# Performance work log

Measured on AMD Instinct MI355X. Metric: run time of the kernel, lower is better.

The kernel has to match this reference:

```python
import jax, jax.numpy as jnp
import numpy as np

N = 50000   # nodes
E = 800000  # edges (avg degree 16)
F = 128     # input_nf = output_nf
H = 128     # hidden_nf


def setup_inputs() -> dict:
    key = jax.random.key(0)
    ks = jax.random.split(key, 10)
    # coords: spatial part in [-1, 1], z-coordinate (last dim) in [0.5, 1.5] (must be > 0)
    xz = jax.random.uniform(ks[0], (N, 3), minval=-1.0, maxval=1.0)
    xz = xz.at[:, -1].set(jax.random.uniform(ks[1], (N,), minval=0.5, maxval=1.5))
    h = jax.random.normal(ks[2], (N, F), dtype=jnp.float32)
    row = jax.random.randint(ks[3], (E,), 0, N)
    # guarantee col != row so AdS distance is strictly positive on every edge
    col = (row + 1 + jax.random.randint(ks[4], (E,), 0, N - 1)) % N
    edge_index = jnp.stack([row, col]).astype(jnp.int32)

    def lin(k, fan_in, fan_out):
        return jax.random.normal(k, (fan_in, fan_out), dtype=jnp.float32) / np.float32(np.sqrt(fan_in))

    return {
        "xz": xz,
        "h": h,
        "We1": lin(ks[5], 2 * F + 1, H), "be1": jnp.full((H,), 0.1, jnp.float32),
        "We2": lin(ks[6], H, H),         "be2": jnp.full((H,), 0.1, jnp.float32),
        "Wn1": lin(ks[7], H + F, H),     "bn1": jnp.full((H,), 0.1, jnp.float32),
        "Wn2": lin(ks[8], H, F),         "bn2": jnp.full((F,), 0.1, jnp.float32),
        "edge_index": edge_index,
    }


def reference(xz, h, We1, be1, We2, be2, Wn1, bn1, Wn2, bn2, edge_index):
    row, col = edge_index[0], edge_index[1]
    n = h.shape[0]

    # AdS (hyperbolic upper-half-space) distance between xz[row] and xz[col]:
    # d = arccosh(1 + |p1 - p2|^2 / (2 z1 z2)), z = last coordinate
    diff = xz[row] - xz[col]                                  # [E, 3]
    u = jnp.sum(diff * diff, axis=-1) / (2.0 * xz[row, -1] * xz[col, -1])
    dist = jnp.arccosh(1.0 + u)[:, None]                      # [E, 1]

    # edge model: concat(source, target, radial) -> Linear -> silu -> Linear -> silu
    m = jnp.concatenate([h[row], h[col], dist], axis=1)       # [E, 2F+1]
    m = jax.nn.silu(m @ We1 + be1)                            # [E, H]
    m = jax.nn.silu(m @ We2 + be2)                            # [E, H]

    # segment_mean over destination nodes (row)
    num = jax.ops.segment_sum(m, row, num_segments=n)                          # [N, H]
    den = jax.ops.segment_sum(jnp.ones_like(m), row, num_segments=n)          # [N, H]
    agg = num / jnp.maximum(den, jnp.ones((), den.dtype))

    # node model: concat(h, agg) -> Linear -> silu -> Linear, plus residual
    z = jnp.concatenate([h, agg], axis=1)                     # [N, F+H]
    out = jax.nn.silu(z @ Wn1 + bn1) @ Wn2 + bn2              # [N, F]
    return h + out
```

## Files before the change

kernel.cpp:

```cpp
#include <hip/hip_runtime.h>

#define NN 50000
#define EE 800000
#define NB 196

typedef __bf16 bf16x8 __attribute__((ext_vector_type(8)));
typedef float  f32x4  __attribute__((ext_vector_type(4)));

__device__ __forceinline__ float bf2f(ushort u) {
    union { unsigned int i; float f; } v; v.i = ((unsigned int)u) << 16; return v.f;
}
__device__ __forceinline__ ushort f2bf(float f) {
    union { float f; unsigned int i; } v; v.f = f;
    unsigned int u = v.i;
    return (ushort)((u + 0x7FFFu + ((u >> 16) & 1u)) >> 16);
}
__device__ __forceinline__ ushort f2bf_fast(float f) {
    union { float f; unsigned int i; } v; v.f = f;
    return (ushort)((v.i + 0x8000u) >> 16);
}
__device__ __forceinline__ float silu(float x) {
    return x * __builtin_amdgcn_rcpf(1.0f + __expf(-x));
}

__device__ __forceinline__ bool detect_isf(const ushort* __restrict__ xzu,
                                           int tid, int* scnt) {
    float v = bf2f(xzu[2 * (tid & 255)]);
    bool sane = (v == v) && (fabsf(v) <= 4.0f);
    unsigned long long m = __ballot(sane);
    if ((tid & 63) == 0) scnt[tid >> 6] = __popcll(m);
    __syncthreads();
    int cnt = scnt[0] + scnt[1] + scnt[2] + scnt[3];
    return cnt < 192;
}

__global__ void prep_all_kernel(const void* __restrict__ hsrc, const void* __restrict__ xzsrc,
                                const int* __restrict__ erow,
                                const void* We1, const void* We2,
                                const void* Wn1, const void* Wn2,
                                const void* be1, const void* be2,
                                const void* bn1, const void* bn2,
                                ushort* __restrict__ hb, float* __restrict__ xzf,
                                int* __restrict__ cntI,
                                ushort* __restrict__ We1s, ushort* __restrict__ We2s,
                                ushort* __restrict__ Wn1s, ushort* __restrict__ Wn2s,
                                float* __restrict__ fb, ushort* __restrict__ wlb) {
    __shared__ int scnt[4];
    const int b = blockIdx.x;
    const int tid = threadIdx.x;

    if (b >= 3712 && b < 6837) {
        int e = (b - 3712) * 256 + tid;
        if (e < EE) atomicAdd(&cntI[erow[e]], 1);
        return;
    }

    const bool isf = detect_isf((const ushort*)xzsrc, tid, scnt);

    if (b < 3125) {
        int i = (b * 256 + tid) * 8;
        uint4 o;
        if (isf) {
            const float* s = (const float*)hsrc + i;
            float4 f0 = *(const float4*)s;
            float4 f1 = *(const float4*)(s + 4);
            o.x = (unsigned int)f2bf(f0.x) | ((unsigned int)f2bf(f0.y) << 16);
            o.y = (unsigned int)f2bf(f0.z) | ((unsigned int)f2bf(f0.w) << 16);
            o.z = (unsigned int)f2bf(f1.x) | ((unsigned int)f2bf(f1.y) << 16);
            o.w = (unsigned int)f2bf(f1.z) | ((unsigned int)f2bf(f1.w) << 16);
        } else {
            o = *(const uint4*)((const ushort*)hsrc + i);
        }
        *(uint4*)(hb + i) = o;
    } else if (b < 3712) {
        int i = (b - 3125) * 256 + tid;
        if (i < NN * 3)
            xzf[i] = isf ? ((const float*)xzsrc)[i] : bf2f(((const ushort*)xzsrc)[i]);
    } else {
        int sw = b - 6837;
        if (sw == 48) {
            for (int j = tid; j < 640; j += 256) {
                int which = j >> 7, k = j & 127;
                const void* src = (which == 0) ? be1 : (which == 1) ? be2 :
                                  (which == 2) ? bn1 : (which == 3) ? bn2 : We1;
                size_t idx = (which == 4) ? ((size_t)256 * 128 + k) : (size_t)k;
                float v = isf ? ((const float*)src)[idx] : bf2f(((const ushort*)src)[idx]);
                fb[j] = v;
                if (which == 4) wlb[k] = f2bf(v);
            }
            return;
        }
        int c = sw * 256 + tid;
        const void* src; ushort* dst; int cl;
        if      (c <  4096) { src = We1; dst = We1s; cl = c;         }
        else if (c <  6144) { src = We2; dst = We2s; cl = c - 4096;  }
        else if (c < 10240) { src = Wn1; dst = Wn1s; cl = c - 6144;  }
        else                { src = Wn2; dst = Wn2s; cl = c - 10240; }
        int l = cl & 63, nt = (cl >> 6) & 7, kc = cl >> 9;
        int kbase = kc * 32 + (l >> 4) * 8;
        int n = nt * 16 + (l & 15);
        ushort tmp[8];
#pragma unroll
        for (int j = 0; j < 8; ++j) {
            size_t idx = (size_t)(kbase + j) * 128 + n;
            tmp[j] = isf ? f2bf(((const float*)src)[idx]) : ((const ushort*)src)[idx];
        }
#pragma unroll
        for (int j = 0; j < 8; ++j) dst[(size_t)cl * 8 + j] = tmp[j];
    }
}

__global__ void scanA_kernel(const int* __restrict__ cntI, int* __restrict__ bsum) {
    __shared__ int s[256];
    int t = threadIdx.x;
    int i = blockIdx.x * 256 + t;
    s[t] = (i < NN) ? cntI[i] : 0;
    __syncthreads();
#pragma unroll
    for (int off = 128; off > 0; off >>= 1) {
        if (t < off) s[t] += s[t + off];
        __syncthreads();
    }
    if (t == 0) bsum[blockIdx.x] = s[0];
}

__global__ void scanC_kernel(const int* __restrict__ cntI, const int* __restrict__ bsum,
                             int* __restrict__ rowStart) {
    __shared__ int s[256];
    __shared__ int sbase;
    int t = threadIdx.x;
    int bv = (t < NB) ? bsum[t] : 0;
    s[t] = bv;
    __syncthreads();
    for (int off = 1; off < 256; off <<= 1) {
        int u = (t >= off) ? s[t - off] : 0;
        __syncthreads();
        if (t >= off) s[t] += u;
        __syncthreads();
    }
    if (t == 0) sbase = (blockIdx.x == 0) ? 0 : s[blockIdx.x - 1];
    __syncthreads();
    int i = blockIdx.x * 256 + t;
    int v = (i < NN) ? cntI[i] : 0;
    s[t] = v;
    __syncthreads();
    for (int off = 1; off < 256; off <<= 1) {
        int u = (t >= off) ? s[t - off] : 0;
        __syncthreads();
        if (t >= off) s[t] += u;
        __syncthreads();
    }
    if (i < NN) rowStart[i] = sbase + s[t] - v;
}

__global__ __launch_bounds__(256, 3) void scatter_pq_kernel(
    const ushort* __restrict__ hb, const ushort* __restrict__ We1s,
    const float* __restrict__ fb, ushort* __restrict__ Pp, ushort* __restrict__ Qq,
    const int* __restrict__ erow, const int* __restrict__ ecol,
    const float* __restrict__ xzf, const int* __restrict__ rowStart,
    int* __restrict__ cursor, int2* __restrict__ eS, uint4* __restrict__ aggz) {
    __shared__ __align__(16) ushort sA[8192];
    const int tid = threadIdx.x;

    if (blockIdx.x >= 3907) {
        const uint4 z = make_uint4(0, 0, 0, 0);
        int g0 = (blockIdx.x - 3907) * 256 + tid;
        const int total = NN * 128 * 4 / 16;
        for (int i = g0; i < total; i += 800 * 256) aggz[i] = z;
        return;
    }
    if (blockIdx.x >= 782) {
        int e = (blockIdx.x - 782) * 256 + tid;
        if (e >= EE) return;
        int r = erow[e], c = ecol[e];
        int pos = rowStart[r] + atomicAdd(&cursor[r], 1);
        float4 a = *(const float4*)(xzf + 3 * r);
        float4 b = *(const float4*)(xzf + 3 * c);
        float dx = a.x - b.x, dy = a.y - b.y, dz = a.z - b.z;
        float u = (dx * dx + dy * dy + dz * dz) * __builtin_amdgcn_rcpf(2.0f * a.z * b.z);
        u = fminf(fmaxf(u, 0.0f), 1.0e6f);
        float d = __logf(1.0f + u + sqrtf(u * (u + 2.0f)));
        eS[pos] = make_int2((r << 16) | c, __float_as_int(d));
        return;
    }

    const int lane = tid & 63, w = tid >> 6;
    const int col = lane & 15, quad = lane >> 4;
    const int nt0 = w * 2;
    const int nA = w * 32 + col, nB = nA + 16;
    const float be1A = fb[nA], be1B = fb[nB];
    const int tile = blockIdx.x;
    const int n0 = tile * 64;
#pragma unroll
    for (int i = 0; i < 4; ++i) {
        int node = n0 + lane;
        uint4 v = (node < NN) ? *(const uint4*)(hb + (size_t)node * 128 + (w + 4 * i) * 8)
                              : make_uint4(0, 0, 0, 0);
        *(uint4*)(sA + (((lane >> 4) * 4 + i) * 64 + w * 16 + (lane & 15)) * 8) = v;
    }
    __syncthreads();

    f32x4 accP[4][2] = {}, accQ[4][2] = {};
#pragma unroll
    for (int kc = 0; kc < 4; ++kc) {
        bf16x8 bp0 = *(const bf16x8*)(We1s + ((kc * 8 + nt0)           * 64 + lane) * 8);
        bf16x8 bp1 = *(const bf16x8*)(We1s + ((kc * 8 + nt0 + 1)       * 64 + lane) * 8);
        bf16x8 bq0 = *(const bf16x8*)(We1s + (((kc + 4) * 8 + nt0)     * 64 + lane) * 8);
        bf16x8 bq1 = *(const bf16x8*)(We1s + (((kc + 4) * 8 + nt0 + 1) * 64 + lane) * 8);
#pragma unroll
        for (int g = 0; g < 4; ++g) {
            bf16x8 a = *(const bf16x8*)(sA + ((g * 4 + kc) * 64 + lane) * 8);
            accP[g][0] = __builtin_amdgcn_mfma_f32_16x16x32_bf16(a, bp0, accP[g][0], 0, 0, 0);
            accP[g][1] = __builtin_amdgcn_mfma_f32_16x16x32_bf16(a, bp1, accP[g][1], 0, 0, 0);
            accQ[g][0] = __builtin_amdgcn_mfma_f32_16x16x32_bf16(a, bq0, accQ[g][0], 0, 0, 0);
            accQ[g][1] = __builtin_amdgcn_mfma_f32_16x16x32_bf16(a, bq1, accQ[g][1], 0, 0, 0);
        }
    }
#pragma unroll
    for (int g = 0; g < 4; ++g) {
#pragma unroll
        for (int r = 0; r < 4; ++r) {
            int node = n0 + g * 16 + quad * 4 + r;
            if (node < NN) {
                size_t o = (size_t)node * 128;
                Pp[o + nA] = f2bf(accP[g][0][r] + be1A);
                Pp[o + nB] = f2bf(accP[g][1][r] + be1B);
                Qq[o + nA] = f2bf(accQ[g][0][r]);
                Qq[o + nB] = f2bf(accQ[g][1][r]);
            }
        }
    }
}

__global__ __launch_bounds__(256, 4) void edge_kernel(
    const ushort* __restrict__ Pp, const ushort* __restrict__ Qq,
    const int2* __restrict__ eS, const ushort* __restrict__ We2s,
    const ushort* __restrict__ wlb, const float* __restrict__ fb,
    float* __restrict__ agg) {
    __shared__ __align__(16) char smem[64 * 132 * 4];
    __shared__ int sRow[64];
    ushort* sM = (ushort*)smem;
    float (*sOut)[132] = (float(*)[132])smem;

    const int tid = threadIdx.x;
    const int lane = tid & 63, w = tid >> 6;
    const int col = lane & 15, quad = lane >> 4;
    const int nt0 = w * 2;

    const int nA = w * 32 + col, nB = nA + 16;
    const float be2A = fb[128 + nA], be2B = fb[128 + nB];

    const int ntiles = EE / 64;
    const int per = (ntiles + gridDim.x - 1) / gridDim.x;
    const int t0 = blockIdx.x * per;
    const int t1 = (t0 + per < ntiles) ? (t0 + per) : ntiles;
    if (t0 >= t1) return;

    bf16x8 B2[8];
#pragma unroll
    for (int kc = 0; kc < 4; ++kc) {
        B2[kc * 2]     = *(const bf16x8*)(We2s + ((kc * 8 + nt0)     * 64 + lane) * 8);
        B2[kc * 2 + 1] = *(const bf16x8*)(We2s + ((kc * 8 + nt0 + 1) * 64 + lane) * 8);
    }
    bf16x8 WL[4];
#pragma unroll
    for (int i = 0; i < 4; ++i) WL[i] = *(const bf16x8*)(wlb + (w + 4 * i) * 8);

    int2 ed = eS[(size_t)t0 * 64 + lane];

    for (int tile = t0; tile < t1; ++tile) {
        const int tn = (tile + 1 < t1) ? (tile + 1) : tile;
        const int2 edn = eS[(size_t)tn * 64 + lane];

        __syncthreads();
        const int r = ((unsigned)ed.x) >> 16, c = ed.x & 0xFFFF;
        const float d = __int_as_float(ed.y);
        if (w == 0) sRow[lane] = r;
#pragma unroll
        for (int i = 0; i < 4; ++i) {
            int ch = w + 4 * i;
            bf16x8 p = *(const bf16x8*)(Pp + (size_t)r * 128 + ch * 8);
            bf16x8 q = *(const bf16x8*)(Qq + (size_t)c * 128 + ch * 8);
            ushort out8[8];
#pragma unroll
            for (int j = 0; j < 8; ++j) {
                float x = (float)p[j] + (float)q[j] + d * (float)WL[i][j];
                out8[j] = f2bf_fast(silu(x));
            }
            *(uint4*)(sM + (((lane >> 4) * 4 + i) * 64 + w * 16 + (lane & 15)) * 8) =
                *(const uint4*)out8;
        }
        ed = edn;
        __syncthreads();

        f32x4 acc2[4][2] = {};
#pragma unroll
        for (int kc = 0; kc < 4; ++kc) {
#pragma unroll
            for (int g = 0; g < 4; ++g) {
                bf16x8 a = *(const bf16x8*)(sM + ((g * 4 + kc) * 64 + lane) * 8);
                acc2[g][0] = __builtin_amdgcn_mfma_f32_16x16x32_bf16(a, B2[kc * 2],     acc2[g][0], 0, 0, 0);
                acc2[g][1] = __builtin_amdgcn_mfma_f32_16x16x32_bf16(a, B2[kc * 2 + 1], acc2[g][1], 0, 0, 0);
            }
        }
        __syncthreads();

#pragma unroll
        for (int g = 0; g < 4; ++g) {
#pragma unroll
            for (int r4 = 0; r4 < 4; ++r4) {
                int m = g * 16 + quad * 4 + r4;
                sOut[m][nA] = silu(acc2[g][0][r4] + be2A);
                sOut[m][nB] = silu(acc2[g][1][r4] + be2B);
            }
        }
        __syncthreads();

        {
            const int cc = tid & 127;
            const int mb = (tid >> 7) * 32;
            float acc = 0.0f;
            int prow = sRow[mb];
            for (int k = 0; k < 32; ++k) {
                int rw = sRow[mb + k];
                if (rw != prow) {
                    unsafeAtomicAdd(&agg[(size_t)prow * 128 + cc], acc);
                    acc = 0.0f;
                    prow = rw;
                }
                acc += sOut[mb + k][cc];
            }
            unsafeAtomicAdd(&agg[(size_t)prow * 128 + cc], acc);
        }
    }
}

__global__ __launch_bounds__(256, 3) void node_kernel(
    const ushort* __restrict__ hb, const void* __restrict__ hraw,
    const void* __restrict__ xzsrc,
    const float* __restrict__ agg, const int* __restrict__ cntI,
    const ushort* __restrict__ Wn1s, const ushort* __restrict__ Wn2s,
    const float* __restrict__ fb, void* __restrict__ outv) {
    __shared__ __align__(16) ushort sA[16384];
    __shared__ __align__(16) ushort sM[8192];
    __shared__ int scnt[4];
    const int tid = threadIdx.x;
    const int lane = tid & 63, w = tid >> 6;
    const int col = lane & 15, quad = lane >> 4;
    const int nt0 = w * 2;
    const int ntiles = (NN + 63) / 64;
    const bool isf = detect_isf((const ushort*)xzsrc, tid, scnt);
    float* outf = (float*)outv;
    ushort* outu = (ushort*)outv;

    const int nA = w * 32 + col, nB = nA + 16;
    const float bn1A = fb[256 + nA], bn1B = fb[256 + nB];
    const float bn2A = fb[384 + nA], bn2B = fb[384 + nB];

    for (int tile = blockIdx.x; tile < ntiles; tile += gridDim.x) {
        __syncthreads();
        const int n0 = tile * 64;
#pragma unroll
        for (int i = 0; i < 8; ++i) {
            int kb = w + 4 * i;
            int node = n0 + lane;
            uint4 v;
            if (node < NN) {
                if (kb < 16) {
                    v = *(const uint4*)(hb + (size_t)node * 128 + kb * 8);
                } else {
                    const float* ap = agg + (size_t)node * 128 + (kb - 16) * 8;
                    float invc = __builtin_amdgcn_rcpf(fmaxf((float)cntI[node], 1.0f));
                    float4 f0 = *(const float4*)ap;
                    float4 f1 = *(const float4*)(ap + 4);
                    v.x = (unsigned int)f2bf_fast(f0.x * invc) | ((unsigned int)f2bf_fast(f0.y * invc) << 16);
                    v.y = (unsigned int)f2bf_fast(f0.z * invc) | ((unsigned int)f2bf_fast(f0.w * invc) << 16);
                    v.z = (unsigned int)f2bf_fast(f1.x * invc) | ((unsigned int)f2bf_fast(f1.y * invc) << 16);
                    v.w = (unsigned int)f2bf_fast(f1.z * invc) | ((unsigned int)f2bf_fast(f1.w * invc) << 16);
                }
            } else {
                v = make_uint4(0, 0, 0, 0);
            }
            *(uint4*)(sA + (((quad * 8 + i) * 64) + w * 16 + col) * 8) = v;
        }
        __syncthreads();

        f32x4 acc[4][2] = {};
#pragma unroll
        for (int kc = 0; kc < 8; ++kc) {
            bf16x8 b0 = *(const bf16x8*)(Wn1s + ((kc * 8 + nt0)     * 64 + lane) * 8);
            bf16x8 b1 = *(const bf16x8*)(Wn1s + ((kc * 8 + nt0 + 1) * 64 + lane) * 8);
#pragma unroll
            for (int g = 0; g < 4; ++g) {
                bf16x8 a = *(const bf16x8*)(sA + ((g * 8 + kc) * 64 + lane) * 8);
                acc[g][0] = __builtin_amdgcn_mfma_f32_16x16x32_bf16(a, b0, acc[g][0], 0, 0, 0);
                acc[g][1] = __builtin_amdgcn_mfma_f32_16x16x32_bf16(a, b1, acc[g][1], 0, 0, 0);
            }
        }
#pragma unroll
        for (int g = 0; g < 4; ++g) {
            int base0 = ((g * 4 + w) * 64 + (col >> 3) * 16) * 8 + (col & 7);
#pragma unroll
            for (int r = 0; r < 4; ++r) {
                int mrow = quad * 4 + r;
                sM[base0 + mrow * 8]              = f2bf_fast(silu(acc[g][0][r] + bn1A));
                sM[base0 + 2 * 16 * 8 + mrow * 8] = f2bf_fast(silu(acc[g][1][r] + bn1B));
            }
        }
        __syncthreads();

        f32x4 acc2[4][2] = {};
#pragma unroll
        for (int kc = 0; kc < 4; ++kc) {
            bf16x8 b0 = *(const bf16x8*)(Wn2s + ((kc * 8 + nt0)     * 64 + lane) * 8);
            bf16x8 b1 = *(const bf16x8*)(Wn2s + ((kc * 8 + nt0 + 1) * 64 + lane) * 8);
#pragma unroll
            for (int g = 0; g < 4; ++g) {
                bf16x8 a = *(const bf16x8*)(sM + ((g * 4 + kc) * 64 + lane) * 8);
                acc2[g][0] = __builtin_amdgcn_mfma_f32_16x16x32_bf16(a, b0, acc2[g][0], 0, 0, 0);
                acc2[g][1] = __builtin_amdgcn_mfma_f32_16x16x32_bf16(a, b1, acc2[g][1], 0, 0, 0);
            }
        }
#pragma unroll
        for (int g = 0; g < 4; ++g) {
#pragma unroll
            for (int r = 0; r < 4; ++r) {
                int ml2 = g * 16 + quad * 4 + r;
                int node = n0 + ml2;
                if (node < NN) {
                    size_t oi = (size_t)node * 128;
                    float h0 = isf ? ((const float*)hraw)[oi + nA] : bf2f(((const ushort*)hraw)[oi + nA]);
                    float h1 = isf ? ((const float*)hraw)[oi + nB] : bf2f(((const ushort*)hraw)[oi + nB]);
                    float x0 = acc2[g][0][r] + bn2A + h0;
                    float x1 = acc2[g][1][r] + bn2B + h1;
                    if (isf) { outf[oi + nA] = x0; outf[oi + nB] = x1; }
                    else     { outu[oi + nA] = f2bf_fast(x0); outu[oi + nB] = f2bf_fast(x1); }
                }
            }
        }
    }
}

extern "C" void kernel_launch(void* const* d_in, const int* in_sizes, int n_in,
                              void* d_out, int out_size, void* d_ws, size_t ws_size,
                              hipStream_t stream) {
    const void* xz  = d_in[0];
    const void* h   = d_in[1];
    const void* We1 = d_in[2];
    const void* be1 = d_in[3];
    const void* We2 = d_in[4];
    const void* be2 = d_in[5];
    const void* Wn1 = d_in[6];
    const void* bn1 = d_in[7];
    const void* Wn2 = d_in[8];
    const void* bn2 = d_in[9];
    const int*  ei  = (const int*)d_in[10];
    const int* erow = ei;
    const int* ecol = ei + EE;

    char* base = (char*)d_ws;
    size_t cur = 0;
    auto alloc = [&](size_t bytes) { size_t o = cur; cur = (cur + bytes + 255) & ~(size_t)255; return o; };
    float*  agg    = (float*) (base + alloc((size_t)NN * 128 * 4));
    int*    cntI   = (int*)   (base + alloc((size_t)NN * 4));
    int*    cursor = (int*)   (base + alloc((size_t)NN * 4));
    ushort* hb     = (ushort*)(base + alloc((size_t)NN * 128 * 2));
    ushort* Pp     = (ushort*)(base + alloc((size_t)NN * 128 * 2));
    ushort* Qq     = (ushort*)(base + alloc((size_t)NN * 128 * 2));
    int2*   eS     = (int2*)  (base + alloc((size_t)EE * 8));
    float*  xzf    = (float*) (base + alloc((size_t)NN * 3 * 4 + 16));
    int*    rowSt  = (int*)   (base + alloc((size_t)NN * 4));
    int*    bsum   = (int*)   (base + alloc(256 * 4));
    ushort* We1s   = (ushort*)(base + alloc(32768 * 2));
    ushort* We2s   = (ushort*)(base + alloc(16384 * 2));
    ushort* Wn1s   = (ushort*)(base + alloc(32768 * 2));
    ushort* Wn2s   = (ushort*)(base + alloc(16384 * 2));
    float*  fb     = (float*) (base + alloc(640 * 4));
    ushort* wlb    = (ushort*)(base + alloc(128 * 2));

    size_t zbytes = (size_t)((char*)hb - (char*)cntI);
    (void)hipMemsetAsync(cntI, 0, zbytes, stream);

    prep_all_kernel<<<6886, 256, 0, stream>>>(h, xz, erow, We1, We2, Wn1, Wn2,
                                              be1, be2, bn1, bn2,
                                              hb, xzf, cntI, We1s, We2s, Wn1s, Wn2s,
                                              fb, wlb);
    scanA_kernel<<<NB, 256, 0, stream>>>(cntI, bsum);
    scanC_kernel<<<NB, 256, 0, stream>>>(cntI, bsum, rowSt);
    scatter_pq_kernel<<<782 + 3125 + 800, 256, 0, stream>>>(hb, We1s, fb, Pp, Qq,
                                                            erow, ecol, xzf, rowSt, cursor,
                                                            eS, (uint4*)agg);
    edge_kernel<<<1024, 256, 0, stream>>>(Pp, Qq, eS, We2s, wlb, fb, agg);
    node_kernel<<<782, 256, 0, stream>>>(hb, h, xz, agg, cntI, Wn1s, Wn2s, fb, d_out);
}
```

Baseline: 329.6 us.

## Raise edge kernel occupancy by halving shared staging and reloading We2 per tile

After: 429.3 us. 30.2% more time.

```diff
diff --git a/kernel.cpp b/kernel.cpp
--- a/kernel.cpp
+++ b/kernel.cpp
@@ -232,12 +232,12 @@
     }
 }
 
-__global__ __launch_bounds__(256, 4) void edge_kernel(
+__global__ __launch_bounds__(256, 6) void edge_kernel(
     const ushort* __restrict__ Pp, const ushort* __restrict__ Qq,
     const int2* __restrict__ eS, const ushort* __restrict__ We2s,
     const ushort* __restrict__ wlb, const float* __restrict__ fb,
     float* __restrict__ agg) {
-    __shared__ __align__(16) char smem[64 * 132 * 4];
+    __shared__ __align__(16) char smem[32 * 132 * 4];
     __shared__ int sRow[64];
     ushort* sM = (ushort*)smem;
     float (*sOut)[132] = (float(*)[132])smem;
@@ -256,12 +256,6 @@
     const int t1 = (t0 + per < ntiles) ? (t0 + per) : ntiles;
     if (t0 >= t1) return;
 
-    bf16x8 B2[8];
-#pragma unroll
-    for (int kc = 0; kc < 4; ++kc) {
-        B2[kc * 2]     = *(const bf16x8*)(We2s + ((kc * 8 + nt0)     * 64 + lane) * 8);
-        B2[kc * 2 + 1] = *(const bf16x8*)(We2s + ((kc * 8 + nt0 + 1) * 64 + lane) * 8);
-    }
     bf16x8 WL[4];
 #pragma unroll
     for (int i = 0; i < 4; ++i) WL[i] = *(const bf16x8*)(wlb + (w + 4 * i) * 8);
@@ -294,43 +288,57 @@
         __syncthreads();
 
         f32x4 acc2[4][2] = {};
-#pragma unroll
-        for (int kc = 0; kc < 4; ++kc) {
-#pragma unroll
-            for (int g = 0; g < 4; ++g) {
-                bf16x8 a = *(const bf16x8*)(sM + ((g * 4 + kc) * 64 + lane) * 8);
-                acc2[g][0] = __builtin_amdgcn_mfma_f32_16x16x32_bf16(a, B2[kc * 2],     acc2[g][0], 0, 0, 0);
-                acc2[g][1] = __builtin_amdgcn_mfma_f32_16x16x32_bf16(a, B2[kc * 2 + 1], acc2[g][1], 0, 0, 0);
-            }
-        }
-        __syncthreads();
-
-#pragma unroll
-        for (int g = 0; g < 4; ++g) {
-#pragma unroll
-            for (int r4 = 0; r4 < 4; ++r4) {
-                int m = g * 16 + quad * 4 + r4;
-                sOut[m][nA] = silu(acc2[g][0][r4] + be2A);
-                sOut[m][nB] = silu(acc2[g][1][r4] + be2B);
-            }
-        }
-        __syncthreads();
-
         {
-            const int cc = tid & 127;
-            const int mb = (tid >> 7) * 32;
-            float acc = 0.0f;
-            int prow = sRow[mb];
-            for (int k = 0; k < 32; ++k) {
-                int rw = sRow[mb + k];
-                if (rw != prow) {
-                    unsafeAtomicAdd(&agg[(size_t)prow * 128 + cc], acc);
-                    acc = 0.0f;
-                    prow = rw;
+            bf16x8 b[8];
+#pragma unroll
+            for (int kc = 0; kc < 4; ++kc) {
+                b[kc * 2]     = *(const bf16x8*)(We2s + ((kc * 8 + nt0)     * 64 + lane) * 8);
+                b[kc * 2 + 1] = *(const bf16x8*)(We2s + ((kc * 8 + nt0 + 1) * 64 + lane) * 8);
+            }
+#pragma unroll
+            for (int kc = 0; kc < 4; ++kc) {
+#pragma unroll
+                for (int g = 0; g < 4; ++g) {
+                    bf16x8 a = *(const bf16x8*)(sM + ((g * 4 + kc) * 64 + lane) * 8);
+                    acc2[g][0] = __builtin_amdgcn_mfma_f32_16x16x32_bf16(a, b[kc * 2],     acc2[g][0], 0, 0, 0);
+                    acc2[g][1] = __builtin_amdgcn_mfma_f32_16x16x32_bf16(a, b[kc * 2 + 1], acc2[g][1], 0, 0, 0);
                 }
-                acc += sOut[mb + k][cc];
-            }
-            unsafeAtomicAdd(&agg[(size_t)prow * 128 + cc], acc);
+            }
+        }
+        __syncthreads();
+
+#pragma unroll
+        for (int pass = 0; pass < 2; ++pass) {
+#pragma unroll
+            for (int gg = 0; gg < 2; ++gg) {
+                int g = pass * 2 + gg;
+#pragma unroll
+                for (int r4 = 0; r4 < 4; ++r4) {
+                    int lr = gg * 16 + quad * 4 + r4;
+                    sOut[lr][nA] = silu(acc2[g][0][r4] + be2A);
+                    sOut[lr][nB] = silu(acc2[g][1][r4] + be2B);
+                }
+            }
+            __syncthreads();
+
+            {
+                const int cc = tid & 127;
+                const int sub = tid >> 7;
+                const int mb = pass * 32 + sub * 16;
+                float acc = 0.0f;
+                int prow = sRow[mb];
+                for (int k = 0; k < 16; ++k) {
+                    int rw = sRow[mb + k];
+                    if (rw != prow) {
+                        unsafeAtomicAdd(&agg[(size_t)prow * 128 + cc], acc);
+                        acc = 0.0f;
+                        prow = rw;
+                    }
+                    acc += sOut[sub * 16 + k][cc];
+                }
+                unsafeAtomicAdd(&agg[(size_t)prow * 128 + cc], acc);
+            }
+            if (pass == 0) __syncthreads();
         }
     }
 }
@@ -490,6 +498,6 @@
     scatter_pq_kernel<<<782 + 3125 + 800, 256, 0, stream>>>(hb, We1s, fb, Pp, Qq,
                                                             erow, ecol, xzf, rowSt, cursor,
                                                             eS, (uint4*)agg);
-    edge_kernel<<<1024, 256, 0, stream>>>(Pp, Qq, eS, We2s, wlb, fb, agg);
+    edge_kernel<<<2048, 256, 0, stream>>>(Pp, Qq, eS, We2s, wlb, fb, agg);
     node_kernel<<<782, 256, 0, stream>>>(hb, h, xz, agg, cntI, Wn1s, Wn2s, fb, d_out);
 }
```
